# Kernel optimization log

Hardware: AMD Instinct MI355X
Metric: run time of the kernel (lower is better)

Reference implementation:

```python
import jax, jax.numpy as jnp
import numpy as np

IN_DIM, OUT_DIM, HIDDEN = 64, 64, 128


def _cell(x, h, c, w_ih, w_hh, b_ih, b_hh):
    # PyTorch LSTM gate order: i, f, g, o
    gates = x @ w_ih.T + b_ih + h @ w_hh.T + b_hh
    i, f, g, o = jnp.split(gates, 4, axis=-1)
    c = jax.nn.sigmoid(f) * c + jax.nn.sigmoid(i) * jnp.tanh(g)
    h = jax.nn.sigmoid(o) * jnp.tanh(c)
    return h, c


def setup_inputs() -> dict:
    key = jax.random.key(0)
    ks = jax.random.split(key, 12)
    B, S = 8192, 128
    s = 1.0 / np.sqrt(HIDDEN)
    u = lambda k, shp: jax.random.uniform(k, shp, jnp.float32, -s, s)
    return {
        "x": jax.random.normal(ks[0], (B, S, IN_DIM), jnp.float32),
        "w_ih0": u(ks[1], (4 * HIDDEN, IN_DIM)),
        "w_hh0": u(ks[2], (4 * HIDDEN, HIDDEN)),
        "b_ih0": u(ks[3], (4 * HIDDEN,)),
        "b_hh0": u(ks[4], (4 * HIDDEN,)),
        "w_ih1": u(ks[5], (4 * HIDDEN, HIDDEN)),
        "w_hh1": u(ks[6], (4 * HIDDEN, HIDDEN)),
        "b_ih1": u(ks[7], (4 * HIDDEN,)),
        "b_hh1": u(ks[8], (4 * HIDDEN,)),
        "w_dec": u(ks[9], (OUT_DIM, HIDDEN)),
        "b_dec": u(ks[10], (OUT_DIM,)),
        "pred_steps": 20,
    }


def reference(x, w_ih0, w_hh0, b_ih0, b_hh0, w_ih1, w_hh1, b_ih1, b_hh1, w_dec, b_dec, pred_steps):
    B = x.shape[0]
    z = jnp.zeros((B, HIDDEN), x.dtype)

    def enc_step(carry, xt):
        h0, c0, h1, c1 = carry
        h0, c0 = _cell(xt, h0, c0, w_ih0, w_hh0, b_ih0, b_hh0)
        h1, c1 = _cell(h0, h1, c1, w_ih1, w_hh1, b_ih1, b_hh1)
        return (h0, c0, h1, c1), None

    carry, _ = jax.lax.scan(enc_step, (z, z, z, z), jnp.swapaxes(x, 0, 1))

    def dec_step(carry, _):
        inp, h0, c0, h1, c1 = carry
        h0, c0 = _cell(inp, h0, c0, w_ih0, w_hh0, b_ih0, b_hh0)
        h1, c1 = _cell(h0, h1, c1, w_ih1, w_hh1, b_ih1, b_hh1)
        p = h1 @ w_dec.T + b_dec
        return (p, h0, c0, h1, c1), p

    _, preds = jax.lax.scan(dec_step, (x[:, -1, :],) + carry, None, length=pred_steps)
    return jnp.swapaxes(preds, 0, 1)  # [B, pred_steps, out_dim]
```

## Files before the change

### kernel.cpp

```cpp
#include <hip/hip_runtime.h>
#include <cstdint>
#include <cstddef>

#define BATCH  8192
#define INDIM  64
#define OUTDIM 64
#define HID    128
#define BT     64
#define NT     512
#define KP     328
#define COLH0  64
#define COLH1  192
#define KB0    6
#define KB1    8
#define KBD    4

#define W0U    0
#define W1U    196608
#define WDU    458752
#define B0F    237568
#define B1F    238080
#define BDF    238592
#define NPACK  238656

typedef unsigned short u16;
typedef __attribute__((ext_vector_type(8))) short bfrag;
typedef __attribute__((ext_vector_type(4))) float facc;

__device__ __forceinline__ u16 f2bf(float x) {
  uint32_t u = __float_as_uint(x);
  return (u16)((u + 0x7fffu + ((u >> 16) & 1u)) >> 16);
}
__device__ __forceinline__ float bf2f(u16 h) {
  return __uint_as_float(((uint32_t)h) << 16);
}
__device__ __forceinline__ float fsig(float x) { return 1.0f / (1.0f + __expf(-x)); }
__device__ __forceinline__ float ftanh(float x) {
  float e = __expf(2.0f * x);
  return 1.0f - 2.0f / (e + 1.0f);
}
__device__ __forceinline__ facc splat4(float v) {
  facc a; a[0] = v; a[1] = v; a[2] = v; a[3] = v; return a;
}

template <int KB>
__device__ __forceinline__ void gemm_block(const u16* __restrict__ wt,
                                           const u16 (&Hhi)[BT][KP],
                                           const u16 (&Hlo)[BT][KP],
                                           int colOff, int c, int g, int ntq,
                                           facc (&acc)[4][4]) {
  bfrag wa[8], wb[8];
#pragma unroll
  for (int t = 0; t < 4; ++t) {
    const u16* p = wt + (((ntq + t) * KB + 0) * 2) * 512;
    wa[t * 2]     = *(const bfrag*)p;
    wa[t * 2 + 1] = *(const bfrag*)(p + 512);
  }
#pragma unroll
  for (int kb = 0; kb < KB; ++kb) {
    bfrag (&cur)[8] = (kb & 1) ? wb : wa;
    bfrag (&nxt)[8] = (kb & 1) ? wa : wb;
    if (kb + 1 < KB) {
#pragma unroll
      for (int t = 0; t < 4; ++t) {
        const u16* p = wt + (((ntq + t) * KB + kb + 1) * 2) * 512;
        nxt[t * 2]     = *(const bfrag*)p;
        nxt[t * 2 + 1] = *(const bfrag*)(p + 512);
      }
    }
    const int k0 = colOff + kb * 32 + g * 8;
    bfrag ah[4], al[4];
#pragma unroll
    for (int mt = 0; mt < 4; ++mt) {
      ah[mt] = *(const bfrag*)&Hhi[mt * 16 + c][k0];
      al[mt] = *(const bfrag*)&Hlo[mt * 16 + c][k0];
    }
#pragma unroll
    for (int mt = 0; mt < 4; ++mt)
#pragma unroll
      for (int t = 0; t < 4; ++t) {
        facc a = acc[mt][t];
        a = __builtin_amdgcn_mfma_f32_16x16x32_bf16(ah[mt], cur[t * 2],     a, 0, 0, 0);
        a = __builtin_amdgcn_mfma_f32_16x16x32_bf16(ah[mt], cur[t * 2 + 1], a, 0, 0, 0);
        a = __builtin_amdgcn_mfma_f32_16x16x32_bf16(al[mt], cur[t * 2],     a, 0, 0, 0);
        acc[mt][t] = a;
      }
  }
}

__global__ __launch_bounds__(NT, 2) void lstm_kernel(
    const float* __restrict__ x, const void* __restrict__ pkv,
    float* __restrict__ out, int S, int P) {
  __shared__ __align__(16) u16 Ahi[BT][KP];
  __shared__ __align__(16) u16 Alo[BT][KP];

  const u16* pku = (const u16*)pkv;
  const float* pkf = (const float*)pkv;

  const int tid = threadIdx.x;
  const int lane = tid & 63;
  const int w = tid >> 6;
  const int c = lane & 15;
  const int g = lane >> 4;
  const int b0 = blockIdx.x * BT;

  for (int i = tid; i < BT * KP; i += NT) {
    (&Ahi[0][0])[i] = 0;
    (&Alo[0][0])[i] = 0;
  }

  float b0r[4], b1r[4];
#pragma unroll
  for (int t = 0; t < 4; ++t) {
    b0r[t] = pkf[B0F + (w * 4 + t) * 16 + c];
    b1r[t] = pkf[B1F + (w * 4 + t) * 16 + c];
  }
  const int ntd = w & 3, mtd = w >> 2;
  const float bdr = pkf[BDF + ntd * 16 + c];

  float c0r[16], c1r[16];
#pragma unroll
  for (int q = 0; q < 16; ++q) { c0r[q] = 0.f; c1r[q] = 0.f; }

  const u16* w0t = pku + W0U + lane * 8;
  const u16* w1t = pku + W1U + lane * 8;
  const u16* wdt = pku + WDU + lane * 8;

  __syncthreads();

  const int T = S + P;
  for (int step = 0; step < T; ++step) {
    if (step < S) {
#pragma unroll
      for (int i = 0; i < 2; ++i) {
        const int q = tid + NT * i;
        const int s = q >> 4, c4 = (q & 15) * 4;
        const float4 v = *(const float4*)(x + ((size_t)(b0 + s) * S + step) * INDIM + c4);
        float vv[4] = {v.x, v.y, v.z, v.w};
        u16 h4[4], l4[4];
#pragma unroll
        for (int qq = 0; qq < 4; ++qq) {
          h4[qq] = f2bf(vv[qq]);
          l4[qq] = f2bf(vv[qq] - bf2f(h4[qq]));
        }
        uint2 hp, lp;
        hp.x = (uint32_t)h4[0] | ((uint32_t)h4[1] << 16);
        hp.y = (uint32_t)h4[2] | ((uint32_t)h4[3] << 16);
        lp.x = (uint32_t)l4[0] | ((uint32_t)l4[1] << 16);
        lp.y = (uint32_t)l4[2] | ((uint32_t)l4[3] << 16);
        *(uint2*)&Ahi[s][c4] = hp;
        *(uint2*)&Alo[s][c4] = lp;
      }
    }
    __syncthreads();

    facc acc[4][4];
#pragma unroll
    for (int mt = 0; mt < 4; ++mt)
#pragma unroll
      for (int t = 0; t < 4; ++t) acc[mt][t] = splat4(b0r[t]);
    gemm_block<KB0>(w0t, Ahi, Alo, 0, c, g, w * 4, acc);
    __syncthreads();
#pragma unroll
    for (int mt = 0; mt < 4; ++mt)
#pragma unroll
      for (int r = 0; r < 4; ++r) {
        float gi = fsig(acc[mt][0][r]);
        float gf = fsig(acc[mt][1][r]);
        float gg = ftanh(acc[mt][2][r]);
        float go = fsig(acc[mt][3][r]);
        float cn = fmaf(gf, c0r[mt * 4 + r], gi * gg);
        c0r[mt * 4 + r] = cn;
        float hv = go * ftanh(cn);
        const int s = mt * 16 + g * 4 + r;
        u16 hh = f2bf(hv);
        Ahi[s][COLH0 + w * 16 + c] = hh;
        Alo[s][COLH0 + w * 16 + c] = f2bf(hv - bf2f(hh));
      }
    __syncthreads();

#pragma unroll
    for (int mt = 0; mt < 4; ++mt)
#pragma unroll
      for (int t = 0; t < 4; ++t) acc[mt][t] = splat4(b1r[t]);
    gemm_block<KB1>(w1t, Ahi, Alo, COLH0, c, g, w * 4, acc);
    __syncthreads();
#pragma unroll
    for (int mt = 0; mt < 4; ++mt)
#pragma unroll
      for (int r = 0; r < 4; ++r) {
        float gi = fsig(acc[mt][0][r]);
        float gf = fsig(acc[mt][1][r]);
        float gg = ftanh(acc[mt][2][r]);
        float go = fsig(acc[mt][3][r]);
        float cn = fmaf(gf, c1r[mt * 4 + r], gi * gg);
        c1r[mt * 4 + r] = cn;
        float hv = go * ftanh(cn);
        const int s = mt * 16 + g * 4 + r;
        u16 hh = f2bf(hv);
        Ahi[s][COLH1 + w * 16 + c] = hh;
        Alo[s][COLH1 + w * 16 + c] = f2bf(hv - bf2f(hh));
      }

    if (step >= S) {
      __syncthreads();
      facc da[2] = {splat4(bdr), splat4(bdr)};
#pragma unroll
      for (int kb = 0; kb < KBD; ++kb) {
        const u16* p = wdt + ((ntd * KBD + kb) * 2) * 512;
        bfrag wbh = *(const bfrag*)p;
        bfrag wbl = *(const bfrag*)(p + 512);
        const int k0 = COLH1 + kb * 32 + g * 8;
#pragma unroll
        for (int mi = 0; mi < 2; ++mi) {
          const int mt = mtd + mi * 2;
          bfrag dah = *(const bfrag*)&Ahi[mt * 16 + c][k0];
          bfrag dal = *(const bfrag*)&Alo[mt * 16 + c][k0];
          da[mi] = __builtin_amdgcn_mfma_f32_16x16x32_bf16(dah, wbh, da[mi], 0, 0, 0);
          da[mi] = __builtin_amdgcn_mfma_f32_16x16x32_bf16(dah, wbl, da[mi], 0, 0, 0);
          da[mi] = __builtin_amdgcn_mfma_f32_16x16x32_bf16(dal, wbh, da[mi], 0, 0, 0);
        }
      }
      const int dstep = step - S;
#pragma unroll
      for (int mi = 0; mi < 2; ++mi) {
        const int mt = mtd + mi * 2;
#pragma unroll
        for (int r = 0; r < 4; ++r) {
          const int s = mt * 16 + g * 4 + r;
          const int o = ntd * 16 + c;
          float pv = da[mi][r];
          out[((size_t)(b0 + s) * P + dstep) * OUTDIM + o] = pv;
          u16 hh = f2bf(pv);
          Ahi[s][o] = hh;
          Alo[s][o] = f2bf(pv - bf2f(hh));
        }
      }
    }
  }
}

__global__ void prepack_kernel(const float* __restrict__ wih0, const float* __restrict__ whh0,
                               const float* __restrict__ bih0, const float* __restrict__ bhh0,
                               const float* __restrict__ wih1, const float* __restrict__ whh1,
                               const float* __restrict__ bih1, const float* __restrict__ bhh1,
                               const float* __restrict__ wdec, const float* __restrict__ bdec,
                               void* __restrict__ pko) {
  int idx = blockIdx.x * blockDim.x + threadIdx.x;
  if (idx >= NPACK) return;
  u16* pu = (u16*)pko;
  float* pf = (float*)pko;
  if (idx < 98304) {
    int nt = idx / 3072, rem = idx % 3072;
    int kb = rem >> 9, q = rem & 511, ln = q >> 3, j = q & 7;
    int n = nt * 16 + (ln & 15);
    int row = ((n >> 4) & 3) * HID + (n >> 6) * 16 + (n & 15);
    int k = kb * 32 + (ln >> 4) * 8 + j;
    float wv = (k < INDIM) ? wih0[row * INDIM + k] : whh0[row * HID + k - INDIM];
    u16 hi = f2bf(wv), lo = f2bf(wv - bf2f(hi));
    int base = W0U + ((nt * KB0 + kb) * 2) * 512;
    pu[base + q] = hi;
    pu[base + 512 + q] = lo;
  } else if (idx < 229376) {
    int r = idx - 98304;
    int nt = r >> 12, rem = r & 4095;
    int kb = rem >> 9, q = rem & 511, ln = q >> 3, j = q & 7;
    int n = nt * 16 + (ln & 15);
    int row = ((n >> 4) & 3) * HID + (n >> 6) * 16 + (n & 15);
    int k = kb * 32 + (ln >> 4) * 8 + j;
    float wv = (k < HID) ? wih1[row * HID + k] : whh1[row * HID + k - HID];
    u16 hi = f2bf(wv), lo = f2bf(wv - bf2f(hi));
    int base = W1U + ((nt * KB1 + kb) * 2) * 512;
    pu[base + q] = hi;
    pu[base + 512 + q] = lo;
  } else if (idx < 237568) {
    int r = idx - 229376;
    int nt = r >> 11, rem = r & 2047;
    int kb = rem >> 9, q = rem & 511, ln = q >> 3, j = q & 7;
    int o = nt * 16 + (ln & 15);
    int k = kb * 32 + (ln >> 4) * 8 + j;
    float wv = wdec[o * HID + k];
    u16 hi = f2bf(wv), lo = f2bf(wv - bf2f(hi));
    int base = WDU + ((nt * KBD + kb) * 2) * 512;
    pu[base + q] = hi;
    pu[base + 512 + q] = lo;
  } else if (idx < 238080) {
    int n = idx - 237568;
    int row = ((n >> 4) & 3) * HID + (n >> 6) * 16 + (n & 15);
    pf[B0F + n] = bih0[row] + bhh0[row];
  } else if (idx < 238592) {
    int n = idx - 238080;
    int row = ((n >> 4) & 3) * HID + (n >> 6) * 16 + (n & 15);
    pf[B1F + n] = bih1[row] + bhh1[row];
  } else {
    int o = idx - 238592;
    pf[BDF + o] = bdec[o];
  }
}

extern "C" void kernel_launch(void* const* d_in, const int* in_sizes, int n_in,
                              void* d_out, int out_size, void* d_ws, size_t ws_size,
                              hipStream_t stream) {
  const float* x    = (const float*)d_in[0];
  const float* wih0 = (const float*)d_in[1];
  const float* whh0 = (const float*)d_in[2];
  const float* bih0 = (const float*)d_in[3];
  const float* bhh0 = (const float*)d_in[4];
  const float* wih1 = (const float*)d_in[5];
  const float* whh1 = (const float*)d_in[6];
  const float* bih1 = (const float*)d_in[7];
  const float* bhh1 = (const float*)d_in[8];
  const float* wdec = (const float*)d_in[9];
  const float* bdec = (const float*)d_in[10];
  float* out = (float*)d_out;

  const int S = in_sizes[0] / (BATCH * INDIM);
  const int P = out_size / (BATCH * OUTDIM);

  prepack_kernel<<<(NPACK + 255) / 256, 256, 0, stream>>>(
      wih0, whh0, bih0, bhh0, wih1, whh1, bih1, bhh1, wdec, bdec, d_ws);

  lstm_kernel<<<BATCH / BT, NT, 0, stream>>>(x, d_ws, out, S, P);
}
```

Baseline: 5.508 ms.

## Prefetch next GEMM's first weight tile across phase boundaries and hoist decoder weight loads

Restructures the weight-fragment double buffering so the buffers persist across the two LSTM layer GEMMs. The last k-block of each GEMM now prefetches the first weight tile of the following GEMM (layer 0 to layer 1, and layer 1 to the next step's layer 0), so the barriers and gate math hide that global load latency instead of exposing it at each GEMM start. Decoder weight fragments are also loaded before the barrier rather than inside the MFMA loop. This keeps more bfrag registers live across the elementwise phases, which adds register pressure under launch_bounds(512,2) and could cause spills.

```diff
diff --git a/kernel.cpp b/kernel.cpp
--- a/kernel.cpp
+++ b/kernel.cpp
@@ -43,48 +43,51 @@
   facc a; a[0] = v; a[1] = v; a[2] = v; a[3] = v; return a;
 }
 
+__device__ __forceinline__ void loadw8(bfrag (&dst)[8], const u16* __restrict__ wt,
+                                       int ntq, int kbn, int kb) {
+#pragma unroll
+  for (int t = 0; t < 4; ++t) {
+    const u16* p = wt + (((ntq + t) * kbn + kb) * 2) * 512;
+    dst[t * 2]     = *(const bfrag*)p;
+    dst[t * 2 + 1] = *(const bfrag*)(p + 512);
+  }
+}
+
+__device__ __forceinline__ void mfma_kb(const bfrag (&wf)[8],
+                                        const u16 (&Hhi)[BT][KP],
+                                        const u16 (&Hlo)[BT][KP],
+                                        int k0, int c, facc (&acc)[4][4]) {
+#pragma unroll
+  for (int mt = 0; mt < 4; ++mt) {
+    const bfrag ah = *(const bfrag*)&Hhi[mt * 16 + c][k0];
+    const bfrag al = *(const bfrag*)&Hlo[mt * 16 + c][k0];
+#pragma unroll
+    for (int t = 0; t < 4; ++t) {
+      facc a = acc[mt][t];
+      a = __builtin_amdgcn_mfma_f32_16x16x32_bf16(ah, wf[t * 2],     a, 0, 0, 0);
+      a = __builtin_amdgcn_mfma_f32_16x16x32_bf16(ah, wf[t * 2 + 1], a, 0, 0, 0);
+      a = __builtin_amdgcn_mfma_f32_16x16x32_bf16(al, wf[t * 2],     a, 0, 0, 0);
+      acc[mt][t] = a;
+    }
+  }
+}
+
 template <int KB>
-__device__ __forceinline__ void gemm_block(const u16* __restrict__ wt,
+__device__ __forceinline__ void gemm_phase(const u16* __restrict__ wt,
+                                           const u16* __restrict__ wtNext, int kbnNext,
                                            const u16 (&Hhi)[BT][KP],
                                            const u16 (&Hlo)[BT][KP],
-                                           int colOff, int c, int g, int ntq,
+                                           int colOff, int c, int gk, int ntq,
+                                           bfrag (&bufA)[8], bfrag (&bufB)[8],
                                            facc (&acc)[4][4]) {
-  bfrag wa[8], wb[8];
-#pragma unroll
-  for (int t = 0; t < 4; ++t) {
-    const u16* p = wt + (((ntq + t) * KB + 0) * 2) * 512;
-    wa[t * 2]     = *(const bfrag*)p;
-    wa[t * 2 + 1] = *(const bfrag*)(p + 512);
-  }
-#pragma unroll
-  for (int kb = 0; kb < KB; ++kb) {
-    bfrag (&cur)[8] = (kb & 1) ? wb : wa;
-    bfrag (&nxt)[8] = (kb & 1) ? wa : wb;
-    if (kb + 1 < KB) {
-#pragma unroll
-      for (int t = 0; t < 4; ++t) {
-        const u16* p = wt + (((ntq + t) * KB + kb + 1) * 2) * 512;
-        nxt[t * 2]     = *(const bfrag*)p;
-        nxt[t * 2 + 1] = *(const bfrag*)(p + 512);
-      }
-    }
-    const int k0 = colOff + kb * 32 + g * 8;
-    bfrag ah[4], al[4];
-#pragma unroll
-    for (int mt = 0; mt < 4; ++mt) {
-      ah[mt] = *(const bfrag*)&Hhi[mt * 16 + c][k0];
-      al[mt] = *(const bfrag*)&Hlo[mt * 16 + c][k0];
-    }
-#pragma unroll
-    for (int mt = 0; mt < 4; ++mt)
-#pragma unroll
-      for (int t = 0; t < 4; ++t) {
-        facc a = acc[mt][t];
-        a = __builtin_amdgcn_mfma_f32_16x16x32_bf16(ah[mt], cur[t * 2],     a, 0, 0, 0);
-        a = __builtin_amdgcn_mfma_f32_16x16x32_bf16(ah[mt], cur[t * 2 + 1], a, 0, 0, 0);
-        a = __builtin_amdgcn_mfma_f32_16x16x32_bf16(al[mt], cur[t * 2],     a, 0, 0, 0);
-        acc[mt][t] = a;
-      }
+  static_assert((KB & 1) == 0, "KB must be even");
+#pragma unroll
+  for (int kb = 0; kb < KB; kb += 2) {
+    loadw8(bufB, wt, ntq, KB, kb + 1);
+    mfma_kb(bufA, Hhi, Hlo, colOff + kb * 32 + gk, c, acc);
+    if (kb + 2 < KB) loadw8(bufA, wt, ntq, KB, kb + 2);
+    else             loadw8(bufA, wtNext, ntq, kbnNext, 0);
+    mfma_kb(bufB, Hhi, Hlo, colOff + (kb + 1) * 32 + gk, c, acc);
   }
 }
 
@@ -101,7 +104,9 @@
   const int lane = tid & 63;
   const int w = tid >> 6;
   const int c = lane & 15;
+  const int gk = (lane >> 4) * 8;
   const int g = lane >> 4;
+  const int ntq = w * 4;
   const int b0 = blockIdx.x * BT;
 
   for (int i = tid; i < BT * KP; i += NT) {
@@ -125,6 +130,9 @@
   const u16* w0t = pku + W0U + lane * 8;
   const u16* w1t = pku + W1U + lane * 8;
   const u16* wdt = pku + WDU + lane * 8;
+
+  bfrag bufA[8], bufB[8];
+  loadw8(bufA, w0t, ntq, KB0, 0);
 
   __syncthreads();
 
@@ -159,7 +167,7 @@
     for (int mt = 0; mt < 4; ++mt)
 #pragma unroll
       for (int t = 0; t < 4; ++t) acc[mt][t] = splat4(b0r[t]);
-    gemm_block<KB0>(w0t, Ahi, Alo, 0, c, g, w * 4, acc);
+    gemm_phase<KB0>(w0t, w1t, KB1, Ahi, Alo, 0, c, gk, ntq, bufA, bufB, acc);
     __syncthreads();
 #pragma unroll
     for (int mt = 0; mt < 4; ++mt)
@@ -183,7 +191,7 @@
     for (int mt = 0; mt < 4; ++mt)
 #pragma unroll
       for (int t = 0; t < 4; ++t) acc[mt][t] = splat4(b1r[t]);
-    gemm_block<KB1>(w1t, Ahi, Alo, COLH0, c, g, w * 4, acc);
+    gemm_phase<KB1>(w1t, w0t, KB0, Ahi, Alo, COLH0, c, gk, ntq, bufA, bufB, acc);
     __syncthreads();
 #pragma unroll
     for (int mt = 0; mt < 4; ++mt)
@@ -203,22 +211,26 @@
       }
 
     if (step >= S) {
+      bfrag wdf[8];
+#pragma unroll
+      for (int kb = 0; kb < KBD; ++kb) {
+        const u16* p = wdt + ((ntd * KBD + kb) * 2) * 512;
+        wdf[kb * 2]     = *(const bfrag*)p;
+        wdf[kb * 2 + 1] = *(const bfrag*)(p + 512);
+      }
       __syncthreads();
       facc da[2] = {splat4(bdr), splat4(bdr)};
 #pragma unroll
       for (int kb = 0; kb < KBD; ++kb) {
-        const u16* p = wdt + ((ntd * KBD + kb) * 2) * 512;
-        bfrag wbh = *(const bfrag*)p;
-        bfrag wbl = *(const bfrag*)(p + 512);
-        const int k0 = COLH1 + kb * 32 + g * 8;
+        const int k0 = COLH1 + kb * 32 + gk;
 #pragma unroll
         for (int mi = 0; mi < 2; ++mi) {
           const int mt = mtd + mi * 2;
           bfrag dah = *(const bfrag*)&Ahi[mt * 16 + c][k0];
           bfrag dal = *(const bfrag*)&Alo[mt * 16 + c][k0];
-          da[mi] = __builtin_amdgcn_mfma_f32_16x16x32_bf16(dah, wbh, da[mi], 0, 0, 0);
-          da[mi] = __builtin_amdgcn_mfma_f32_16x16x32_bf16(dah, wbl, da[mi], 0, 0, 0);
-          da[mi] = __builtin_amdgcn_mfma_f32_16x16x32_bf16(dal, wbh, da[mi], 0, 0, 0);
+          da[mi] = __builtin_amdgcn_mfma_f32_16x16x32_bf16(dah, wdf[kb * 2],     da[mi], 0, 0, 0);
+          da[mi] = __builtin_amdgcn_mfma_f32_16x16x32_bf16(dah, wdf[kb * 2 + 1], da[mi], 0, 0, 0);
+          da[mi] = __builtin_amdgcn_mfma_f32_16x16x32_bf16(dal, wdf[kb * 2],     da[mi], 0, 0, 0);
         }
       }
       const int dstep = step - S;
```

Result: no change. 5.538 ms (+0.5%).
